# Optimization experiments

Hardware: AMD Instinct MI355X
Metric: run time of the kernel (lower is better)

## Reference

```python
import jax, jax.numpy as jnp
import numpy as np

N_DRUG, N_PROT = 20000, 8000
D_DRUG, D_PROT = 300, 1280
HIDDEN, OUT = 512, 5
N_EDGE, N_LBL = 500000, 200000


def setup_inputs() -> dict:
    key = jax.random.key(0)
    ks = jax.random.split(key, 12)
    inp = {
        "x_drug": jax.random.normal(ks[0], (N_DRUG, D_DRUG), dtype=jnp.float32),
        "x_prot": jax.random.normal(ks[1], (N_PROT, D_PROT), dtype=jnp.float32),
        "edge_src": jax.random.randint(ks[2], (N_EDGE,), 0, N_DRUG, dtype=jnp.int32),
        "edge_dst": jax.random.randint(ks[3], (N_EDGE,), 0, N_PROT, dtype=jnp.int32),
        "lbl_src": jax.random.randint(ks[4], (N_LBL,), 0, N_DRUG, dtype=jnp.int32),
        "lbl_dst": jax.random.randint(ks[5], (N_LBL,), 0, N_PROT, dtype=jnp.int32),
        # SAGEConv params: lin_l (on aggregated src msgs, with bias), lin_r (on dst, no bias)
        "W_l": jax.random.normal(ks[6], (HIDDEN, D_DRUG), dtype=jnp.float32) / np.sqrt(D_DRUG),
        "b_l": jnp.zeros((HIDDEN,), dtype=jnp.float32),
        "W_r": jax.random.normal(ks[7], (HIDDEN, D_PROT), dtype=jnp.float32) / np.sqrt(D_PROT),
        # final edge classifier Linear(D_DRUG + HIDDEN, OUT)
        "W_lin": jax.random.normal(ks[8], (OUT, D_DRUG + HIDDEN), dtype=jnp.float32) / np.sqrt(D_DRUG + HIDDEN),
        "b_lin": jnp.zeros((OUT,), dtype=jnp.float32),
    }
    return inp


def reference(x_drug, x_prot, edge_src, edge_dst, lbl_src, lbl_dst,
              W_l, b_l, W_r, W_lin, b_lin):
    # --- bipartite SAGEConv((drug, protein)) with default mean aggregation ---
    msg = x_drug[edge_src]                                   # [E, D_DRUG] gather
    agg = jax.ops.segment_sum(msg, edge_dst, num_segments=N_PROT)   # [N_PROT, D_DRUG]
    cnt = jax.ops.segment_sum(jnp.ones((edge_dst.shape[0],), jnp.float32),
                              edge_dst, num_segments=N_PROT)
    mean = agg / jnp.clip(cnt, 1.0, None)[:, None]           # mean over in-neighbors
    prot_emb_all = mean @ W_l.T + b_l + x_prot @ W_r.T       # [N_PROT, HIDDEN]

    # --- gather endpoints for labeled edges, concat, linear ---
    drug_emb = x_drug[lbl_src]                               # [L, D_DRUG]
    prot_emb = prot_emb_all[lbl_dst]                         # [L, HIDDEN]
    edge_emb = jnp.concatenate([drug_emb, prot_emb], axis=1) # [L, D_DRUG+HIDDEN]
    return edge_emb @ W_lin.T + b_lin                        # [L, OUT]
```

## Files before the change

kernel.cpp:

```cpp
#include <hip/hip_runtime.h>

#define N_DRUG 20000
#define N_PROT 8000
#define D_DRUG 300
#define D_PROT 1280
#define HIDDEN 512
#define OUT_D  5
#define N_EDGE 500000
#define N_LBL  200000
#define W_LIN_LD (D_DRUG + HIDDEN)
#define CAP    96

__global__ void k_small(const float* __restrict__ W_l, const float* __restrict__ W_r,
                        const float* __restrict__ W_lin, const float* __restrict__ b_l,
                        float* __restrict__ A, float* __restrict__ B, float* __restrict__ c) {
    int t = blockIdx.x * blockDim.x + threadIdx.x;
    int h0 = blockIdx.y * 64;
    const int nA = OUT_D * D_DRUG;
    const int nB = OUT_D * D_PROT;
    if (t < nA) {
        int o = t / D_DRUG, k = t - o * D_DRUG;
        const float* wp = W_lin + o * W_LIN_LD + D_DRUG + h0;
        const float* wl = W_l + (size_t)h0 * D_DRUG + k;
        float s = 0.f;
#pragma unroll 4
        for (int h = 0; h < 64; ++h) s += wp[h] * wl[h * D_DRUG];
        atomicAdd(&A[t], s);
    } else if (t < nA + nB) {
        int u = t - nA;
        int o = u / D_PROT, k = u - o * D_PROT;
        const float* wp = W_lin + o * W_LIN_LD + D_DRUG + h0;
        const float* wr = W_r + (size_t)h0 * D_PROT + k;
        float s = 0.f;
#pragma unroll 4
        for (int h = 0; h < 64; ++h) s += wp[h] * wr[h * D_PROT];
        atomicAdd(&B[u], s);
    } else if (t < nA + nB + OUT_D) {
        int o = t - nA - nB;
        const float* wp = W_lin + o * W_LIN_LD + D_DRUG + h0;
        float s = 0.f;
        for (int h = 0; h < 64; ++h) s += wp[h] * b_l[h0 + h];
        atomicAdd(&c[o], s);
    }
}

__global__ void k_drug(const float* __restrict__ x_drug, const float* __restrict__ A,
                       const float* __restrict__ W_lin,
                       float* __restrict__ P_A, float* __restrict__ drugO) {
    int gid = blockIdx.x * blockDim.x + threadIdx.x;
    int row = gid >> 4;
    int sub = threadIdx.x & 15;
    if (row >= N_DRUG) return;
    const float4* xr = (const float4*)(x_drug + (size_t)row * D_DRUG);
    float acc[10];
#pragma unroll
    for (int i = 0; i < 10; ++i) acc[i] = 0.f;
    for (int k = sub; k < D_DRUG / 4; k += 16) {
        float4 x = xr[k];
#pragma unroll
        for (int o = 0; o < OUT_D; ++o) {
            float4 a = ((const float4*)(A + o * D_DRUG))[k];
            acc[o] += x.x * a.x + x.y * a.y + x.z * a.z + x.w * a.w;
            float4 w = ((const float4*)(W_lin + o * W_LIN_LD))[k];
            acc[5 + o] += x.x * w.x + x.y * w.y + x.z * w.z + x.w * w.w;
        }
    }
#pragma unroll
    for (int i = 0; i < 10; ++i) {
        float v = acc[i];
        for (int m = 8; m; m >>= 1) v += __shfl_xor(v, m, 64);
        acc[i] = v;
    }
    if (sub < OUT_D) {
        P_A[row * OUT_D + sub]   = acc[sub];
        drugO[row * OUT_D + sub] = acc[5 + sub];
    }
}

__global__ void k_place(const int* __restrict__ edge_src, const int* __restrict__ edge_dst,
                        const float* __restrict__ P_A,
                        int* __restrict__ bucket, int* __restrict__ cnt,
                        float* __restrict__ agg5) {
    int e = blockIdx.x * blockDim.x + threadIdx.x;
    if (e >= N_EDGE) return;
    int s = edge_src[e], d = edge_dst[e];
    int r = atomicAdd(&cnt[d], 1);
    if (r < CAP) {
        bucket[(size_t)d * CAP + r] = s;
    } else {
        const float* p = &P_A[s * OUT_D];
#pragma unroll
        for (int o = 0; o < OUT_D; ++o) atomicAdd(&agg5[d * OUT_D + o], p[o]);
    }
}

__global__ void k_prot(const float* __restrict__ x_prot, const float* __restrict__ B,
                       const float* __restrict__ c, const float* __restrict__ agg5,
                       const int* __restrict__ cnt, const int* __restrict__ bucket,
                       const float* __restrict__ P_A, float* __restrict__ protO) {
    int wave = (blockIdx.x * blockDim.x + threadIdx.x) >> 6;
    int lane = threadIdx.x & 63;
    if (wave >= N_PROT) return;
    const float4* xr = (const float4*)(x_prot + (size_t)wave * D_PROT);
    float acc[10];
#pragma unroll
    for (int i = 0; i < 10; ++i) acc[i] = 0.f;
    for (int k = lane; k < D_PROT / 4; k += 64) {
        float4 x = xr[k];
#pragma unroll
        for (int o = 0; o < OUT_D; ++o) {
            float4 b = ((const float4*)(B + o * D_PROT))[k];
            acc[o] += x.x * b.x + x.y * b.y + x.z * b.z + x.w * b.w;
        }
    }
    int deg = cnt[wave];
    int m = deg < CAP ? deg : CAP;
    const int* br = &bucket[(size_t)wave * CAP];
    for (int j = lane; j < m; j += 64) {
        const float* p = &P_A[br[j] * OUT_D];
#pragma unroll
        for (int o = 0; o < OUT_D; ++o) acc[5 + o] += p[o];
    }
#pragma unroll
    for (int i = 0; i < 10; ++i) {
        float v = acc[i];
        for (int off = 32; off; off >>= 1) v += __shfl_xor(v, off, 64);
        acc[i] = v;
    }
    if (lane < OUT_D) {
        float invc = 1.f / fmaxf((float)deg, 1.f);
        protO[wave * OUT_D + lane] =
            (acc[5 + lane] + agg5[wave * OUT_D + lane]) * invc + acc[lane] + c[lane];
    }
}

__global__ void k_final(const int* __restrict__ lbl_src, const int* __restrict__ lbl_dst,
                        const float* __restrict__ drugO, const float* __restrict__ protO,
                        const float* __restrict__ b_lin, float* __restrict__ out) {
    int l = blockIdx.x * blockDim.x + threadIdx.x;
    if (l >= N_LBL) return;
    int s = lbl_src[l], d = lbl_dst[l];
    const float* dr = &drugO[s * OUT_D];
    const float* pr = &protO[d * OUT_D];
    float* op = &out[(size_t)l * OUT_D];
    op[0] = dr[0] + pr[0] + b_lin[0];
    op[1] = dr[1] + pr[1] + b_lin[1];
    op[2] = dr[2] + pr[2] + b_lin[2];
    op[3] = dr[3] + pr[3] + b_lin[3];
    op[4] = dr[4] + pr[4] + b_lin[4];
}

extern "C" void kernel_launch(void* const* d_in, const int* in_sizes, int n_in,
                              void* d_out, int out_size, void* d_ws, size_t ws_size,
                              hipStream_t stream) {
    const float* x_drug   = (const float*)d_in[0];
    const float* x_prot   = (const float*)d_in[1];
    const int*   edge_src = (const int*)d_in[2];
    const int*   edge_dst = (const int*)d_in[3];
    const int*   lbl_src  = (const int*)d_in[4];
    const int*   lbl_dst  = (const int*)d_in[5];
    const float* W_l      = (const float*)d_in[6];
    const float* b_l      = (const float*)d_in[7];
    const float* W_r      = (const float*)d_in[8];
    const float* W_lin    = (const float*)d_in[9];
    const float* b_lin    = (const float*)d_in[10];
    float* out = (float*)d_out;

    char* ws = (char*)d_ws;
    int*   cnt    = (int*)  (ws + 0);
    float* agg5   = (float*)(ws + 32000);
    float* A      = (float*)(ws + 192000);
    float* B      = (float*)(ws + 198016);
    float* c      = (float*)(ws + 223616);
    float* P_A    = (float*)(ws + 224000);
    float* drugO  = (float*)(ws + 624000);
    float* protO  = (float*)(ws + 1024000);
    int*   bucket = (int*)  (ws + 1184000);

    hipMemsetAsync(ws, 0, 224000, stream);

    dim3 gs((OUT_D * (D_DRUG + D_PROT) + OUT_D + 255) / 256, HIDDEN / 64);
    k_small<<<gs, 256, 0, stream>>>(W_l, W_r, W_lin, b_l, A, B, c);
    k_drug<<<(N_DRUG * 16 + 255) / 256, 256, 0, stream>>>(x_drug, A, W_lin, P_A, drugO);
    k_place<<<(N_EDGE + 255) / 256, 256, 0, stream>>>(edge_src, edge_dst, P_A, bucket, cnt, agg5);
    k_prot<<<(N_PROT * 64 + 255) / 256, 256, 0, stream>>>(x_prot, B, c, agg5, cnt, bucket, P_A, protO);
    k_final<<<(N_LBL + 255) / 256, 256, 0, stream>>>(lbl_src, lbl_dst, drugO, protO, b_lin, out);
}
```

Baseline: 176.3 us.

## Merge independent kernels into combined launches and move edge bucketing earlier

The weight-folding work and the edge bucketing now run in one launch, and the drug and protein projections run together in a second launch, so independent work shares the GPU instead of running back to back. Because bucketing no longer needs P_A, overflow edges (beyond CAP, now raised to 128) go into a global overflow list that a separate gather kernel scans, replacing the per-edge float atomics. Five launches become four plus a smaller memset. The trade-off is an extra pass over protO and a linear scan of the overflow list for high-degree nodes.

```diff
diff --git a/kernel.cpp b/kernel.cpp
--- a/kernel.cpp
+++ b/kernel.cpp
@@ -8,130 +8,155 @@
 #define OUT_D  5
 #define N_EDGE 500000
 #define N_LBL  200000
-#define W_LIN_LD (D_DRUG + HIDDEN)
-#define CAP    96
-
-__global__ void k_small(const float* __restrict__ W_l, const float* __restrict__ W_r,
-                        const float* __restrict__ W_lin, const float* __restrict__ b_l,
-                        float* __restrict__ A, float* __restrict__ B, float* __restrict__ c) {
-    int t = blockIdx.x * blockDim.x + threadIdx.x;
-    int h0 = blockIdx.y * 64;
-    const int nA = OUT_D * D_DRUG;
-    const int nB = OUT_D * D_PROT;
-    if (t < nA) {
-        int o = t / D_DRUG, k = t - o * D_DRUG;
-        const float* wp = W_lin + o * W_LIN_LD + D_DRUG + h0;
-        const float* wl = W_l + (size_t)h0 * D_DRUG + k;
-        float s = 0.f;
+#define WLD    812
+#define CAP    128
+#define OVF_MAX 65536
+
+__global__ void k_stage1(const float* __restrict__ W_l, const float* __restrict__ W_r,
+                         const float* __restrict__ W_lin, const float* __restrict__ b_l,
+                         const int* __restrict__ edge_src, const int* __restrict__ edge_dst,
+                         float* __restrict__ A, float* __restrict__ B, float* __restrict__ c,
+                         int* __restrict__ cnt, int* __restrict__ novf,
+                         int* __restrict__ bucket, int* __restrict__ ovf) {
+    int b = blockIdx.x;
+    if (b < 248) {
+        int t  = (b % 31) * 256 + threadIdx.x;
+        int h0 = (b / 31) * 64;
+        const int nA = OUT_D * D_DRUG;
+        const int nB = OUT_D * D_PROT;
+        if (t < nA) {
+            int o = t / D_DRUG, k = t - o * D_DRUG;
+            const float* wp = W_lin + o * WLD + D_DRUG + h0;
+            const float* wl = W_l + (size_t)h0 * D_DRUG + k;
+            float s = 0.f;
 #pragma unroll 4
-        for (int h = 0; h < 64; ++h) s += wp[h] * wl[h * D_DRUG];
-        atomicAdd(&A[t], s);
-    } else if (t < nA + nB) {
-        int u = t - nA;
-        int o = u / D_PROT, k = u - o * D_PROT;
-        const float* wp = W_lin + o * W_LIN_LD + D_DRUG + h0;
-        const float* wr = W_r + (size_t)h0 * D_PROT + k;
-        float s = 0.f;
+            for (int h = 0; h < 64; ++h) s += wp[h] * wl[h * D_DRUG];
+            atomicAdd(&A[t], s);
+        } else if (t < nA + nB) {
+            int u = t - nA;
+            int o = u / D_PROT, k = u - o * D_PROT;
+            const float* wp = W_lin + o * WLD + D_DRUG + h0;
+            const float* wr = W_r + (size_t)h0 * D_PROT + k;
+            float s = 0.f;
 #pragma unroll 4
-        for (int h = 0; h < 64; ++h) s += wp[h] * wr[h * D_PROT];
-        atomicAdd(&B[u], s);
-    } else if (t < nA + nB + OUT_D) {
-        int o = t - nA - nB;
-        const float* wp = W_lin + o * W_LIN_LD + D_DRUG + h0;
-        float s = 0.f;
-        for (int h = 0; h < 64; ++h) s += wp[h] * b_l[h0 + h];
-        atomicAdd(&c[o], s);
-    }
-}
-
-__global__ void k_drug(const float* __restrict__ x_drug, const float* __restrict__ A,
-                       const float* __restrict__ W_lin,
-                       float* __restrict__ P_A, float* __restrict__ drugO) {
-    int gid = blockIdx.x * blockDim.x + threadIdx.x;
-    int row = gid >> 4;
-    int sub = threadIdx.x & 15;
-    if (row >= N_DRUG) return;
-    const float4* xr = (const float4*)(x_drug + (size_t)row * D_DRUG);
-    float acc[10];
-#pragma unroll
-    for (int i = 0; i < 10; ++i) acc[i] = 0.f;
-    for (int k = sub; k < D_DRUG / 4; k += 16) {
-        float4 x = xr[k];
+            for (int h = 0; h < 64; ++h) s += wp[h] * wr[h * D_PROT];
+            atomicAdd(&B[u], s);
+        } else if (t < nA + nB + OUT_D) {
+            int o = t - nA - nB;
+            const float* wp = W_lin + o * WLD + D_DRUG + h0;
+            float s = 0.f;
+            for (int h = 0; h < 64; ++h) s += wp[h] * b_l[h0 + h];
+            atomicAdd(&c[o], s);
+        }
+    } else {
+        int base = (b - 248) * 2048 + threadIdx.x;
+#pragma unroll
+        for (int i = 0; i < 8; ++i) {
+            int e = base + i * 256;
+            if (e < N_EDGE) {
+                int s = edge_src[e], d = edge_dst[e];
+                int r = atomicAdd(&cnt[d], 1);
+                if (r < CAP) {
+                    bucket[d * CAP + r] = s;
+                } else {
+                    int o = atomicAdd(novf, 1);
+                    if (o < OVF_MAX) { ovf[2 * o] = d; ovf[2 * o + 1] = s; }
+                }
+            }
+        }
+    }
+}
+
+__global__ void k_stage2(const float* __restrict__ x_drug, const float* __restrict__ x_prot,
+                         const float* __restrict__ A, const float* __restrict__ B,
+                         const float* __restrict__ c, const float* __restrict__ W_lin,
+                         float* __restrict__ P_A, float* __restrict__ drugO,
+                         float* __restrict__ protO) {
+    int b = blockIdx.x;
+    if (b < 1250) {
+        int gid = b * 256 + threadIdx.x;
+        int row = gid >> 4;
+        int sub = threadIdx.x & 15;
+        const float4* xr = (const float4*)(x_drug + (size_t)row * D_DRUG);
+        float acc[10];
+#pragma unroll
+        for (int i = 0; i < 10; ++i) acc[i] = 0.f;
+        for (int k = sub; k < D_DRUG / 4; k += 16) {
+            float4 x = xr[k];
+#pragma unroll
+            for (int o = 0; o < OUT_D; ++o) {
+                float4 a = ((const float4*)(A + o * D_DRUG))[k];
+                acc[o] += x.x * a.x + x.y * a.y + x.z * a.z + x.w * a.w;
+                float4 w = ((const float4*)(W_lin + o * WLD))[k];
+                acc[5 + o] += x.x * w.x + x.y * w.y + x.z * w.z + x.w * w.w;
+            }
+        }
+#pragma unroll
+        for (int i = 0; i < 10; ++i) {
+            float v = acc[i];
+            for (int m = 8; m; m >>= 1) v += __shfl_xor(v, m, 64);
+            acc[i] = v;
+        }
+        if (sub < OUT_D) {
+            P_A[row * OUT_D + sub]   = acc[sub];
+            drugO[row * OUT_D + sub] = acc[5 + sub];
+        }
+    } else {
+        int wave = ((b - 1250) * 256 + threadIdx.x) >> 6;
+        int lane = threadIdx.x & 63;
+        const float4* xr = (const float4*)(x_prot + (size_t)wave * D_PROT);
+        float acc[OUT_D] = {0.f, 0.f, 0.f, 0.f, 0.f};
+        for (int k = lane; k < D_PROT / 4; k += 64) {
+            float4 x = xr[k];
+#pragma unroll
+            for (int o = 0; o < OUT_D; ++o) {
+                float4 bb = ((const float4*)(B + o * D_PROT))[k];
+                acc[o] += x.x * bb.x + x.y * bb.y + x.z * bb.z + x.w * bb.w;
+            }
+        }
 #pragma unroll
         for (int o = 0; o < OUT_D; ++o) {
-            float4 a = ((const float4*)(A + o * D_DRUG))[k];
-            acc[o] += x.x * a.x + x.y * a.y + x.z * a.z + x.w * a.w;
-            float4 w = ((const float4*)(W_lin + o * W_LIN_LD))[k];
-            acc[5 + o] += x.x * w.x + x.y * w.y + x.z * w.z + x.w * w.w;
-        }
-    }
-#pragma unroll
-    for (int i = 0; i < 10; ++i) {
-        float v = acc[i];
-        for (int m = 8; m; m >>= 1) v += __shfl_xor(v, m, 64);
-        acc[i] = v;
-    }
-    if (sub < OUT_D) {
-        P_A[row * OUT_D + sub]   = acc[sub];
-        drugO[row * OUT_D + sub] = acc[5 + sub];
-    }
-}
-
-__global__ void k_place(const int* __restrict__ edge_src, const int* __restrict__ edge_dst,
-                        const float* __restrict__ P_A,
-                        int* __restrict__ bucket, int* __restrict__ cnt,
-                        float* __restrict__ agg5) {
-    int e = blockIdx.x * blockDim.x + threadIdx.x;
-    if (e >= N_EDGE) return;
-    int s = edge_src[e], d = edge_dst[e];
-    int r = atomicAdd(&cnt[d], 1);
-    if (r < CAP) {
-        bucket[(size_t)d * CAP + r] = s;
-    } else {
-        const float* p = &P_A[s * OUT_D];
-#pragma unroll
-        for (int o = 0; o < OUT_D; ++o) atomicAdd(&agg5[d * OUT_D + o], p[o]);
-    }
-}
-
-__global__ void k_prot(const float* __restrict__ x_prot, const float* __restrict__ B,
-                       const float* __restrict__ c, const float* __restrict__ agg5,
-                       const int* __restrict__ cnt, const int* __restrict__ bucket,
-                       const float* __restrict__ P_A, float* __restrict__ protO) {
+            float v = acc[o];
+            for (int off = 32; off; off >>= 1) v += __shfl_xor(v, off, 64);
+            acc[o] = v;
+        }
+        if (lane < OUT_D) protO[wave * OUT_D + lane] = acc[lane] + c[lane];
+    }
+}
+
+__global__ void k_gather(const int* __restrict__ cnt, const int* __restrict__ novf,
+                         const int* __restrict__ bucket, const int* __restrict__ ovf,
+                         const float* __restrict__ P_A, float* __restrict__ protO) {
     int wave = (blockIdx.x * blockDim.x + threadIdx.x) >> 6;
     int lane = threadIdx.x & 63;
     if (wave >= N_PROT) return;
-    const float4* xr = (const float4*)(x_prot + (size_t)wave * D_PROT);
-    float acc[10];
-#pragma unroll
-    for (int i = 0; i < 10; ++i) acc[i] = 0.f;
-    for (int k = lane; k < D_PROT / 4; k += 64) {
-        float4 x = xr[k];
-#pragma unroll
-        for (int o = 0; o < OUT_D; ++o) {
-            float4 b = ((const float4*)(B + o * D_PROT))[k];
-            acc[o] += x.x * b.x + x.y * b.y + x.z * b.z + x.w * b.w;
-        }
-    }
     int deg = cnt[wave];
     int m = deg < CAP ? deg : CAP;
-    const int* br = &bucket[(size_t)wave * CAP];
+    float acc[OUT_D] = {0.f, 0.f, 0.f, 0.f, 0.f};
+    const int* br = &bucket[wave * CAP];
     for (int j = lane; j < m; j += 64) {
         const float* p = &P_A[br[j] * OUT_D];
 #pragma unroll
-        for (int o = 0; o < OUT_D; ++o) acc[5 + o] += p[o];
-    }
-#pragma unroll
-    for (int i = 0; i < 10; ++i) {
-        float v = acc[i];
+        for (int o = 0; o < OUT_D; ++o) acc[o] += p[o];
+    }
+    if (deg > CAP) {
+        int nv = *novf; if (nv > OVF_MAX) nv = OVF_MAX;
+        for (int j = lane; j < nv; j += 64) {
+            if (ovf[2 * j] == wave) {
+                const float* p = &P_A[ovf[2 * j + 1] * OUT_D];
+#pragma unroll
+                for (int o = 0; o < OUT_D; ++o) acc[o] += p[o];
+            }
+        }
+    }
+#pragma unroll
+    for (int o = 0; o < OUT_D; ++o) {
+        float v = acc[o];
         for (int off = 32; off; off >>= 1) v += __shfl_xor(v, off, 64);
-        acc[i] = v;
-    }
-    if (lane < OUT_D) {
-        float invc = 1.f / fmaxf((float)deg, 1.f);
-        protO[wave * OUT_D + lane] =
-            (acc[5 + lane] + agg5[wave * OUT_D + lane]) * invc + acc[lane] + c[lane];
-    }
+        acc[o] = v;
+    }
+    if (lane < OUT_D)
+        protO[wave * OUT_D + lane] += acc[lane] / fmaxf((float)deg, 1.f);
 }
 
 __global__ void k_final(const int* __restrict__ lbl_src, const int* __restrict__ lbl_dst,
@@ -168,21 +193,21 @@
 
     char* ws = (char*)d_ws;
     int*   cnt    = (int*)  (ws + 0);
-    float* agg5   = (float*)(ws + 32000);
-    float* A      = (float*)(ws + 192000);
-    float* B      = (float*)(ws + 198016);
-    float* c      = (float*)(ws + 223616);
-    float* P_A    = (float*)(ws + 224000);
-    float* drugO  = (float*)(ws + 624000);
-    float* protO  = (float*)(ws + 1024000);
-    int*   bucket = (int*)  (ws + 1184000);
-
-    hipMemsetAsync(ws, 0, 224000, stream);
-
-    dim3 gs((OUT_D * (D_DRUG + D_PROT) + OUT_D + 255) / 256, HIDDEN / 64);
-    k_small<<<gs, 256, 0, stream>>>(W_l, W_r, W_lin, b_l, A, B, c);
-    k_drug<<<(N_DRUG * 16 + 255) / 256, 256, 0, stream>>>(x_drug, A, W_lin, P_A, drugO);
-    k_place<<<(N_EDGE + 255) / 256, 256, 0, stream>>>(edge_src, edge_dst, P_A, bucket, cnt, agg5);
-    k_prot<<<(N_PROT * 64 + 255) / 256, 256, 0, stream>>>(x_prot, B, c, agg5, cnt, bucket, P_A, protO);
+    int*   novf   = (int*)  (ws + 32000);
+    float* A      = (float*)(ws + 32016);
+    float* B      = (float*)(ws + 38016);
+    float* c      = (float*)(ws + 63616);
+    float* P_A    = (float*)(ws + 64000);
+    float* drugO  = (float*)(ws + 464000);
+    float* protO  = (float*)(ws + 864000);
+    int*   bucket = (int*)  (ws + 1024000);
+    int*   ovf    = (int*)  (ws + 5120000);
+
+    hipMemsetAsync(ws, 0, 63648, stream);
+    k_stage1<<<493, 256, 0, stream>>>(W_l, W_r, W_lin, b_l, edge_src, edge_dst,
+                                      A, B, c, cnt, novf, bucket, ovf);
+    k_stage2<<<3250, 256, 0, stream>>>(x_drug, x_prot, A, B, c, W_lin,
+                                       P_A, drugO, protO);
+    k_gather<<<(N_PROT * 64) / 256, 256, 0, stream>>>(cnt, novf, bucket, ovf, P_A, protO);
     k_final<<<(N_LBL + 255) / 256, 256, 0, stream>>>(lbl_src, lbl_dst, drugO, protO, b_lin, out);
 }
```

Measured after the change: 165.0 us. 1.07x faster.
